# Kernel tuning notes

Hardware: AMD Instinct MI355X
Metric: run time of the kernel (lower is better)

Reference implementation:

```python
import jax, jax.numpy as jnp
import numpy as np

B, T, C, H = 4, 2048, 1024, 16

def setup_inputs() -> dict:
    key = jax.random.key(0)
    k1, k2, k3, k4, k5 = jax.random.split(key, 5)
    s = 1.0 / np.sqrt(C)
    return {
        "x": jax.random.normal(k1, (B, T, C), dtype=jnp.float32),
        "w_attn": jax.random.normal(k2, (C, 3 * C), dtype=jnp.float32) * s,
        "b_attn": jax.random.normal(k3, (3 * C,), dtype=jnp.float32) * 0.02,
        "w_proj": jax.random.normal(k4, (C, C), dtype=jnp.float32) * s,
        "b_proj": jax.random.normal(k5, (C,), dtype=jnp.float32) * 0.02,
    }

def reference(x, w_attn, b_attn, w_proj, b_proj):
    Bx, Tx, Cx = x.shape
    hd = Cx // H  # head_size
    qkv = x @ w_attn + b_attn                      # [B,T,3C]
    q, k, v = jnp.split(qkv, 3, axis=2)
    # [B,T,C] -> [B,H,T,hd]
    def heads(t):
        return t.reshape(Bx, Tx, H, hd).transpose(0, 2, 1, 3)
    q, k, v = heads(q), heads(k), heads(v)
    scale = hd ** -0.5
    scores = jnp.einsum("bhqd,bhkd->bhqk", q, k) * scale  # [B,H,T,T]
    causal = jnp.tril(jnp.ones((Tx, Tx), dtype=bool))
    scores = jnp.where(causal[None, None], scores, -jnp.inf)
    probs = jax.nn.softmax(scores, axis=-1)
    attn = jnp.einsum("bhqk,bhkd->bhqd", probs, v)  # [B,H,T,hd]
    attn = attn.transpose(0, 2, 1, 3).reshape(Bx, Tx, Cx)
    return attn @ w_proj + b_proj
```

## Files before the change

### kernel.cpp

```cpp
#include <hip/hip_runtime.h>
#include <hip/hip_bf16.h>

#define BATCH 4
#define TSEQ  2048
#define CDIM  1024
#define NHEAD 16
#define HDIM  64
#define C3    3072
#define MROWS (BATCH * TSEQ)

#define QSCALE 0.18033688011112f

typedef short bf16x8 __attribute__((ext_vector_type(8)));
typedef short short8 __attribute__((ext_vector_type(8)));
typedef __bf16 bf16v8 __attribute__((ext_vector_type(8)));
typedef float f32x4 __attribute__((ext_vector_type(4)));

#define AS1 __attribute__((address_space(1)))
#define AS3 __attribute__((address_space(3)))

__device__ __forceinline__ short f2bf(float x) {
    unsigned int u = __builtin_bit_cast(unsigned int, x);
    u += 0x7fffu + ((u >> 16) & 1u);
    return (short)(u >> 16);
}

__device__ __forceinline__ unsigned int cvtpk(float lo, float hi) {
    unsigned int r;
    asm("v_cvt_pk_bf16_f32 %0, %1, %2" : "=v"(r) : "v"(lo), "v"(hi));
    return r;
}

__device__ __forceinline__ f32x4 mfma16(bf16x8 a, bf16x8 b, f32x4 c) {
    return __builtin_amdgcn_mfma_f32_16x16x32_bf16(
        __builtin_bit_cast(bf16v8, a), __builtin_bit_cast(bf16v8, b), c, 0, 0, 0);
}

__global__ void f32_to_bf16_kernel(const float* __restrict__ in,
                                   short* __restrict__ out, int n8) {
    int i = blockIdx.x * blockDim.x + threadIdx.x;
    if (i >= n8) return;
    float4 a = ((const float4*)in)[2 * i];
    float4 b = ((const float4*)in)[2 * i + 1];
    short8 o;
    o[0] = f2bf(a.x); o[1] = f2bf(a.y); o[2] = f2bf(a.z); o[3] = f2bf(a.w);
    o[4] = f2bf(b.x); o[5] = f2bf(b.y); o[6] = f2bf(b.z); o[7] = f2bf(b.w);
    ((short8*)out)[i] = o;
}

__global__ void transpose_f32_bf16_kernel(const float* __restrict__ in,
                                          short* __restrict__ out,
                                          int K, int N, int qcols, float qs) {
    __shared__ float tile[32][33];
    const int n0 = blockIdx.x * 32, k0 = blockIdx.y * 32;
    const int tx = threadIdx.x, ty = threadIdx.y;
#pragma unroll
    for (int j = 0; j < 4; ++j)
        tile[ty + j * 8][tx] = in[(size_t)(k0 + ty + j * 8) * N + n0 + tx];
    __syncthreads();
#pragma unroll
    for (int j = 0; j < 4; ++j) {
        const int n = n0 + ty + j * 8;
        const float s = (n < qcols) ? qs : 1.0f;
        out[(size_t)n * K + k0 + tx] = f2bf(tile[tx][ty + j * 8] * s);
    }
}

template <typename OutT, int WAVES_M, int WAVES_N, int BN>
__global__ __launch_bounds__(512, 4) void gemm3_kernel(
    const short* __restrict__ A, const short* __restrict__ Bt,
    const float* __restrict__ bias, OutT* __restrict__ out,
    int M, int N, int K, int qcols, float qs) {
    constexpr int BM = 128;
    constexpr int MF = BM / (WAVES_M * 16);
    constexpr int NF = BN / (WAVES_N * 16);
    constexpr int BLOADS = BN / 128;
    __shared__ alignas(16) short Ab[3][BM * 32];
    __shared__ alignas(16) short Bb[3][BN * 32];

    const int tid = threadIdx.x;
    const int lane = tid & 63;
    const int w = tid >> 6;
    const int wm = w / WAVES_N;
    const int wn = w % WAVES_N;

    const int nwg = gridDim.x * gridDim.y;
    const int lid = blockIdx.y * gridDim.x + blockIdx.x;
    const int swz = (lid & 7) * (nwg >> 3) + (lid >> 3);
    const int m0 = (swz / gridDim.x) * BM;
    const int n0 = (swz % gridDim.x) * BN;

    const int NT = K >> 5;

    const int fr = lane & 15;
    const int ch = lane >> 4;

    f32x4 acc[MF][NF] = {};

    const int rA  = tid >> 2;
    const int lcA = (tid & 3) ^ ((rA >> 1) & 3);
    const short* gA = A + (size_t)(m0 + rA) * K + lcA * 8;
    const short* gB[BLOADS];
#pragma unroll
    for (int i = 0; i < BLOADS; ++i) {
        const int s = tid + i * 512;
        const int r = s >> 2;
        const int lc = (s & 3) ^ ((r >> 1) & 3);
        gB[i] = Bt + (size_t)(n0 + r) * K + lc * 8;
    }

    int aoff[MF], boff[NF];
#pragma unroll
    for (int f = 0; f < MF; ++f) {
        const int r = wm * (BM / WAVES_M) + f * 16 + fr;
        aoff[f] = r * 32 + (ch ^ ((r >> 1) & 3)) * 8;
    }
#pragma unroll
    for (int f = 0; f < NF; ++f) {
        const int r = wn * (BN / WAVES_N) + f * 16 + fr;
        boff[f] = r * 32 + (ch ^ ((r >> 1) & 3)) * 8;
    }

#define GSTAGE(buf, kt)                                                          \
    do {                                                                         \
        __builtin_amdgcn_global_load_lds((const AS1 void*)(gA + (kt)),           \
            (AS3 void*)&Ab[buf][w * 512], 16, 0, 0);                             \
        _Pragma("unroll")                                                        \
        for (int i = 0; i < BLOADS; ++i)                                         \
            __builtin_amdgcn_global_load_lds((const AS1 void*)(gB[i] + (kt)),    \
                (AS3 void*)&Bb[buf][i * 4096 + w * 512], 16, 0, 0);              \
    } while (0)

#define GITER(BUF, T)                                                            \
    do {                                                                         \
        if constexpr (BLOADS == 2) {                                             \
            asm volatile("s_waitcnt vmcnt(3)" ::: "memory");                     \
        } else {                                                                 \
            asm volatile("s_waitcnt vmcnt(2)" ::: "memory");                     \
        }                                                                        \
        __builtin_amdgcn_s_barrier();                                            \
        __builtin_amdgcn_sched_barrier(0);                                       \
        bf16x8 af[MF], bfv[NF];                                                  \
        _Pragma("unroll")                                                        \
        for (int f = 0; f < MF; ++f)                                             \
            af[f] = *(const bf16x8*)&Ab[BUF][aoff[f]];                           \
        _Pragma("unroll")                                                        \
        for (int f = 0; f < NF; ++f)                                             \
            bfv[f] = *(const bf16x8*)&Bb[BUF][boff[f]];                          \
        const int ktn = (((T) + 2 < NT) ? ((T) + 2) : 0) * 32;                   \
        GSTAGE((BUF + 2) % 3, ktn);                                              \
        _Pragma("unroll")                                                        \
        for (int mf = 0; mf < MF; ++mf)                                          \
            _Pragma("unroll")                                                    \
            for (int nf = 0; nf < NF; ++nf)                                      \
                acc[mf][nf] = mfma16(af[mf], bfv[nf], acc[mf][nf]);              \
    } while (0)

    GSTAGE(0, 0);
    GSTAGE(1, 32);

    int t = 0;
    for (; t + 3 <= NT; t += 3) {
        GITER(0, t);
        GITER(1, t + 1);
        GITER(2, t + 2);
    }
    if (t < NT) { GITER(0, t); ++t; }
    if (t < NT) { GITER(1, t); }
#undef GITER
#undef GSTAGE

    const int r0 = (lane >> 4) * 4;
    const int cn = lane & 15;
#pragma unroll
    for (int mf = 0; mf < MF; ++mf) {
#pragma unroll
        for (int nf = 0; nf < NF; ++nf) {
            const int col = n0 + wn * (BN / WAVES_N) + nf * 16 + cn;
            const float bv = bias[col] * ((col < qcols) ? qs : 1.0f);
#pragma unroll
            for (int r = 0; r < 4; ++r) {
                const int row = m0 + wm * (BM / WAVES_M) + mf * 16 + r0 + r;
                const float v = acc[mf][nf][r] + bv;
                if constexpr (sizeof(OutT) == 2)
                    out[(size_t)row * N + col] = (OutT)f2bf(v);
                else
                    out[(size_t)row * N + col] = (OutT)v;
            }
        }
    }
}

template <int BUF>
__device__ __forceinline__ void attn_iter(
    int KB, int niter, int qrow, int w, int cn, int g, int kg8,
    int krow, int kx0, int kx1, int skv, int sd0,
    const short* kgl, size_t ksrc, const short* vbase,
    short (*klds)[64 * 64], short (*vt)[64 * 72],
    const bf16x8 (&qf)[2][2], f32x4 (&ao)[2][4], f32x4 (&ao4)[2],
    const bf16x8& vones) {

    const int kvb = KB * 64;
    const bool pf = (KB + 1 < niter);

    bf16x8 r0, r1;
    if (pf) {
        r0 = *(const bf16x8*)(vbase + (size_t)(kvb + 64 + skv) * C3 + sd0);
        r1 = *(const bf16x8*)(vbase + (size_t)(kvb + 64 + skv + 1) * C3 + sd0);
        const short* kn = kgl + ksrc + (size_t)(kvb + 64) * C3;
        __builtin_amdgcn_global_load_lds((const AS1 void*)kn,
            (AS3 void*)&klds[BUF ^ 1][w * 512], 16, 0, 0);
        __builtin_amdgcn_global_load_lds((const AS1 void*)(kn + (size_t)32 * C3),
            (AS3 void*)&klds[BUF ^ 1][2048 + w * 512], 16, 0, 0);
    }

    if (kvb <= qrow + 31) {
        bf16x8 kf[4][2];
#pragma unroll
        for (int t = 0; t < 4; ++t) {
            const int rb = t * 1024 + krow;
            kf[t][0] = *(const bf16x8*)&klds[BUF][rb + kx0];
            kf[t][1] = *(const bf16x8*)&klds[BUF][rb + kx1];
        }

        bf16x8 vf[2][4];
#pragma unroll
        for (int c = 0; c < 2; ++c)
#pragma unroll
            for (int dt = 0; dt < 4; ++dt)
                vf[c][dt] = *(const bf16x8*)&vt[BUF][(dt * 16 + cn) * 72 + c * 32 + kg8];

#pragma unroll
        for (int qt = 0; qt < 2; ++qt) {
            const int qrow16 = qrow + qt * 16;

            f32x4 s[4] = {};
#pragma unroll
            for (int t = 0; t < 4; ++t) {
                s[t] = mfma16(kf[t][0], qf[qt][0], s[t]);
                s[t] = mfma16(kf[t][1], qf[qt][1], s[t]);
            }

            const bool maskIter = (kvb + 63 > qrow16);
            float p[4][4];
            if (maskIter) {
#pragma unroll
                for (int t = 0; t < 4; ++t)
#pragma unroll
                    for (int r = 0; r < 4; ++r) {
                        const int kv = kvb + t * 16 + 4 * g + r;
                        const int q  = qrow16 + cn;
                        float e = exp2f(s[t][r]);
                        p[t][r] = (kv > q) ? 0.f : e;
                    }
            } else {
#pragma unroll
                for (int t = 0; t < 4; ++t)
#pragma unroll
                    for (int r = 0; r < 4; ++r)
                        p[t][r] = exp2f(s[t][r]);
            }

            unsigned int wq[8];
#pragma unroll
            for (int t = 0; t < 4; ++t) {
                wq[t * 2 + 0] = cvtpk(p[t][0], p[t][1]);
                wq[t * 2 + 1] = cvtpk(p[t][2], p[t][3]);
            }

#pragma unroll
            for (int c = 0; c < 2; ++c) {
                union { unsigned int u[4]; bf16x8 v; } pu;
                unsigned int p0 = wq[4 * c + 0], p2 = wq[4 * c + 2];
                asm("v_permlane32_swap_b32 %0, %1" : "+v"(p0), "+v"(p2));
                asm("v_permlane16_swap_b32 %0, %1" : "+v"(p0), "+v"(p2));
                pu.u[0] = p0; pu.u[2] = p2;
                unsigned int p1 = wq[4 * c + 1], p3 = wq[4 * c + 3];
                asm("v_permlane32_swap_b32 %0, %1" : "+v"(p1), "+v"(p3));
                asm("v_permlane16_swap_b32 %0, %1" : "+v"(p1), "+v"(p3));
                pu.u[1] = p1; pu.u[3] = p3;
#pragma unroll
                for (int dt = 0; dt < 4; ++dt)
                    ao[qt][dt] = mfma16(pu.v, vf[c][dt], ao[qt][dt]);
                ao4[qt] = mfma16(pu.v, vones, ao4[qt]);
            }
        }
    }

    if (pf) {
#pragma unroll
        for (int i = 0; i < 8; ++i) {
            unsigned int pk = (unsigned short)r0[i] | ((unsigned int)(unsigned short)r1[i] << 16);
            *(unsigned int*)&vt[BUF ^ 1][(sd0 + i) * 72 + skv] = pk;
        }
    }
    __syncthreads();
}

__global__ __launch_bounds__(256) void attn_kernel(const short* __restrict__ qkv,
                                                   short* __restrict__ attn_out) {
    __shared__ short vt[2][64 * 72];
    __shared__ short klds[2][64 * 64];

    const int tid = threadIdx.x;
    const int lane = tid & 63;
    const int w = tid >> 6;

    const int bid = blockIdx.x;
    const int swz = (bid & 7) * 64 + (bid >> 3);
    const int bh = swz >> 3;
    const int pairp = swz & 7;
    const int b = bh >> 4;
    const int h = bh & 15;

    const size_t base = (size_t)b * TSEQ * C3 + (size_t)h * HDIM;
    const int cn = lane & 15;
    const int g = lane >> 4;
    const int kg8 = g * 8;

    const bf16x8 vones = {0x3F80, 0x3F80, 0x3F80, 0x3F80,
                          0x3F80, 0x3F80, 0x3F80, 0x3F80};

    const short* kgl = qkv + base + 1024;
    const size_t ksrc = (size_t)(w * 8 + (lane >> 3)) * C3 + ((lane & 7) ^ (lane >> 3)) * 8;
    const int cnl = cn & 7;
    const int krow = cn * 64;
    const int kx0 = ((g ^ cnl) * 8);
    const int kx1 = (((g ^ 4) ^ cnl) * 8);

    const int skv = (tid & 31) * 2;
    const int sd0 = (tid >> 5) * 8;
    const short* vbase = qkv + base + 2048;

    for (int pass = 0; pass < 2; ++pass) {
        const int qi = pass ? pairp : (15 - pairp);
        const int q0 = qi * 128;
        const int qrow = q0 + w * 32;
        const int niter = 2 * qi + 2;

        bf16x8 qf[2][2];
#pragma unroll
        for (int qt = 0; qt < 2; ++qt)
#pragma unroll
            for (int ks = 0; ks < 2; ++ks)
                qf[qt][ks] = *(const bf16x8*)(qkv + base +
                    (size_t)(qrow + qt * 16 + cn) * C3 + ks * 32 + kg8);

        f32x4 ao[2][4] = {};
        f32x4 ao4[2] = {};

        {
            __builtin_amdgcn_global_load_lds((const AS1 void*)(kgl + ksrc),
                                             (AS3 void*)&klds[0][w * 512], 16, 0, 0);
            __builtin_amdgcn_global_load_lds((const AS1 void*)(kgl + ksrc + (size_t)32 * C3),
                                             (AS3 void*)&klds[0][2048 + w * 512], 16, 0, 0);
            bf16x8 r0 = *(const bf16x8*)(vbase + (size_t)skv * C3 + sd0);
            bf16x8 r1 = *(const bf16x8*)(vbase + (size_t)(skv + 1) * C3 + sd0);
#pragma unroll
            for (int i = 0; i < 8; ++i) {
                unsigned int pk = (unsigned short)r0[i] | ((unsigned int)(unsigned short)r1[i] << 16);
                *(unsigned int*)&vt[0][(sd0 + i) * 72 + skv] = pk;
            }
        }
        __syncthreads();

        int kb = 0;
        for (; kb + 2 <= niter; kb += 2) {
            attn_iter<0>(kb,     niter, qrow, w, cn, g, kg8, krow, kx0, kx1,
                         skv, sd0, kgl, ksrc, vbase, klds, vt, qf, ao, ao4, vones);
            attn_iter<1>(kb + 1, niter, qrow, w, cn, g, kg8, krow, kx0, kx1,
                         skv, sd0, kgl, ksrc, vbase, klds, vt, qf, ao, ao4, vones);
        }

#pragma unroll
        for (int qt = 0; qt < 2; ++qt) {
#pragma unroll
            for (int r = 0; r < 4; ++r) {
                const float lr = 1.0f / ao4[qt][r];
                const int q = qrow + qt * 16 + 4 * g + r;
#pragma unroll
                for (int dt = 0; dt < 4; ++dt)
                    attn_out[(size_t)(b * TSEQ + q) * CDIM + h * HDIM + dt * 16 + cn] =
                        f2bf(ao[qt][dt][r] * lr);
            }
        }
        __syncthreads();
    }
}

extern "C" void kernel_launch(void* const* d_in, const int* in_sizes, int n_in,
                              void* d_out, int out_size, void* d_ws, size_t ws_size,
                              hipStream_t stream) {
    const float* x      = (const float*)d_in[0];
    const float* w_attn = (const float*)d_in[1];
    const float* b_attn = (const float*)d_in[2];
    const float* w_proj = (const float*)d_in[3];
    const float* b_proj = (const float*)d_in[4];
    float* out = (float*)d_out;

    char* ws = (char*)d_ws;
    short* x_bf   = (short*)ws;
    short* wqkvT  = (short*)(ws + (16u << 20));
    short* wprojT = (short*)(ws + (22u << 20));
    short* qkv    = (short*)(ws + (24u << 20));

    f32_to_bf16_kernel<<<(MROWS * CDIM / 8 + 255) / 256, 256, 0, stream>>>(x, x_bf, MROWS * CDIM / 8);
    transpose_f32_bf16_kernel<<<dim3(C3 / 32, CDIM / 32), dim3(32, 8), 0, stream>>>(
        w_attn, wqkvT, CDIM, C3, CDIM, QSCALE);
    transpose_f32_bf16_kernel<<<dim3(CDIM / 32, CDIM / 32), dim3(32, 8), 0, stream>>>(
        w_proj, wprojT, CDIM, CDIM, 0, 1.0f);

    gemm3_kernel<short, 2, 4, 256><<<dim3(C3 / 256, MROWS / 128), 512, 0, stream>>>(
        x_bf, wqkvT, b_attn, qkv, MROWS, C3, CDIM, CDIM, QSCALE);

    attn_kernel<<<dim3(512), 256, 0, stream>>>(qkv, x_bf);

    gemm3_kernel<float, 4, 2, 128><<<dim3(CDIM / 128, MROWS / 128), 512, 0, stream>>>(
        x_bf, wprojT, b_proj, out, MROWS, CDIM, CDIM, 0, 1.0f);
}
```

Baseline: 182.1 us.

## Split attention q-tile pairs into separate blocks with XCD-aware causal balancing

```diff
diff --git a/kernel.cpp b/kernel.cpp
--- a/kernel.cpp
+++ b/kernel.cpp
@@ -15,9 +15,16 @@
 typedef short short8 __attribute__((ext_vector_type(8)));
 typedef __bf16 bf16v8 __attribute__((ext_vector_type(8)));
 typedef float f32x4 __attribute__((ext_vector_type(4)));
+typedef unsigned int u32x4v __attribute__((ext_vector_type(4)));
 
 #define AS1 __attribute__((address_space(1)))
 #define AS3 __attribute__((address_space(3)))
+
+#if __has_builtin(__builtin_amdgcn_exp2f)
+#define EXP2F(x) __builtin_amdgcn_exp2f(x)
+#else
+#define EXP2F(x) exp2f(x)
+#endif
 
 __device__ __forceinline__ short f2bf(float x) {
     unsigned int u = __builtin_bit_cast(unsigned int, x);
@@ -34,6 +41,27 @@
 __device__ __forceinline__ f32x4 mfma16(bf16x8 a, bf16x8 b, f32x4 c) {
     return __builtin_amdgcn_mfma_f32_16x16x32_bf16(
         __builtin_bit_cast(bf16v8, a), __builtin_bit_cast(bf16v8, b), c, 0, 0, 0);
+}
+
+__device__ __forceinline__ void vpack_write(short* dst, const bf16x8& r0,
+                                            const bf16x8& r1, int skv, int sd0) {
+#if __has_builtin(__builtin_amdgcn_perm)
+    u32x4v a = __builtin_bit_cast(u32x4v, r0);
+    u32x4v b = __builtin_bit_cast(u32x4v, r1);
+#pragma unroll
+    for (int wd = 0; wd < 4; ++wd) {
+        unsigned int lo = __builtin_amdgcn_perm(b[wd], a[wd], 0x05040100u);
+        unsigned int hi = __builtin_amdgcn_perm(b[wd], a[wd], 0x07060302u);
+        *(unsigned int*)&dst[(sd0 + 2 * wd + 0) * 72 + skv] = lo;
+        *(unsigned int*)&dst[(sd0 + 2 * wd + 1) * 72 + skv] = hi;
+    }
+#else
+#pragma unroll
+    for (int i = 0; i < 8; ++i) {
+        unsigned int pk = (unsigned short)r0[i] | ((unsigned int)(unsigned short)r1[i] << 16);
+        *(unsigned int*)&dst[(sd0 + i) * 72 + skv] = pk;
+    }
+#endif
 }
 
 __global__ void f32_to_bf16_kernel(const float* __restrict__ in,
@@ -250,7 +278,7 @@
                     for (int r = 0; r < 4; ++r) {
                         const int kv = kvb + t * 16 + 4 * g + r;
                         const int q  = qrow16 + cn;
-                        float e = exp2f(s[t][r]);
+                        float e = EXP2F(s[t][r]);
                         p[t][r] = (kv > q) ? 0.f : e;
                     }
             } else {
@@ -258,7 +286,7 @@
                 for (int t = 0; t < 4; ++t)
 #pragma unroll
                     for (int r = 0; r < 4; ++r)
-                        p[t][r] = exp2f(s[t][r]);
+                        p[t][r] = EXP2F(s[t][r]);
             }
 
             unsigned int wq[8];
@@ -287,18 +315,12 @@
         }
     }
 
-    if (pf) {
-#pragma unroll
-        for (int i = 0; i < 8; ++i) {
-            unsigned int pk = (unsigned short)r0[i] | ((unsigned int)(unsigned short)r1[i] << 16);
-            *(unsigned int*)&vt[BUF ^ 1][(sd0 + i) * 72 + skv] = pk;
-        }
-    }
+    if (pf) vpack_write(vt[BUF ^ 1], r0, r1, skv, sd0);
     __syncthreads();
 }
 
-__global__ __launch_bounds__(256) void attn_kernel(const short* __restrict__ qkv,
-                                                   short* __restrict__ attn_out) {
+__global__ __launch_bounds__(256, 4) void attn_kernel(const short* __restrict__ qkv,
+                                                      short* __restrict__ attn_out) {
     __shared__ short vt[2][64 * 72];
     __shared__ short klds[2][64 * 64];
 
@@ -307,9 +329,12 @@
     const int w = tid >> 6;
 
     const int bid = blockIdx.x;
-    const int swz = (bid & 7) * 64 + (bid >> 3);
-    const int bh = swz >> 3;
-    const int pairp = swz & 7;
+    const int xcd = bid & 7;
+    const int cu  = (bid >> 3) & 31;
+    const int k   = bid >> 8;
+    const int j   = cu >> 3;
+    const int qi  = (k & 1) ? (15 - 2 * j - (k >> 1)) : (2 * j + (k >> 1));
+    const int bh  = xcd * 8 + (cu & 7);
     const int b = bh >> 4;
     const int h = bh & 15;
 
@@ -332,59 +357,51 @@
     const int sd0 = (tid >> 5) * 8;
     const short* vbase = qkv + base + 2048;
 
-    for (int pass = 0; pass < 2; ++pass) {
-        const int qi = pass ? pairp : (15 - pairp);
-        const int q0 = qi * 128;
-        const int qrow = q0 + w * 32;
-        const int niter = 2 * qi + 2;
-
-        bf16x8 qf[2][2];
-#pragma unroll
-        for (int qt = 0; qt < 2; ++qt)
-#pragma unroll
-            for (int ks = 0; ks < 2; ++ks)
-                qf[qt][ks] = *(const bf16x8*)(qkv + base +
-                    (size_t)(qrow + qt * 16 + cn) * C3 + ks * 32 + kg8);
-
-        f32x4 ao[2][4] = {};
-        f32x4 ao4[2] = {};
-
-        {
-            __builtin_amdgcn_global_load_lds((const AS1 void*)(kgl + ksrc),
-                                             (AS3 void*)&klds[0][w * 512], 16, 0, 0);
-            __builtin_amdgcn_global_load_lds((const AS1 void*)(kgl + ksrc + (size_t)32 * C3),
-                                             (AS3 void*)&klds[0][2048 + w * 512], 16, 0, 0);
-            bf16x8 r0 = *(const bf16x8*)(vbase + (size_t)skv * C3 + sd0);
-            bf16x8 r1 = *(const bf16x8*)(vbase + (size_t)(skv + 1) * C3 + sd0);
-#pragma unroll
-            for (int i = 0; i < 8; ++i) {
-                unsigned int pk = (unsigned short)r0[i] | ((unsigned int)(unsigned short)r1[i] << 16);
-                *(unsigned int*)&vt[0][(sd0 + i) * 72 + skv] = pk;
-            }
+    const int q0 = qi * 128;
+    const int qrow = q0 + w * 32;
+    const int niter = 2 * qi + 2;
+
+    bf16x8 qf[2][2];
+#pragma unroll
+    for (int qt = 0; qt < 2; ++qt)
+#pragma unroll
+        for (int ks = 0; ks < 2; ++ks)
+            qf[qt][ks] = *(const bf16x8*)(qkv + base +
+                (size_t)(qrow + qt * 16 + cn) * C3 + ks * 32 + kg8);
+
+    f32x4 ao[2][4] = {};
+    f32x4 ao4[2] = {};
+
+    {
+        __builtin_amdgcn_global_load_lds((const AS1 void*)(kgl + ksrc),
+                                         (AS3 void*)&klds[0][w * 512], 16, 0, 0);
+        __builtin_amdgcn_global_load_lds((const AS1 void*)(kgl + ksrc + (size_t)32 * C3),
+                                         (AS3 void*)&klds[0][2048 + w * 512], 16, 0, 0);
+        bf16x8 r0 = *(const bf16x8*)(vbase + (size_t)skv * C3 + sd0);
+        bf16x8 r1 = *(const bf16x8*)(vbase + (size_t)(skv + 1) * C3 + sd0);
+        vpack_write(vt[0], r0, r1, skv, sd0);
+    }
+    __syncthreads();
+
+    int kb = 0;
+    for (; kb + 2 <= niter; kb += 2) {
+        attn_iter<0>(kb,     niter, qrow, w, cn, g, kg8, krow, kx0, kx1,
+                     skv, sd0, kgl, ksrc, vbase, klds, vt, qf, ao, ao4, vones);
+        attn_iter<1>(kb + 1, niter, qrow, w, cn, g, kg8, krow, kx0, kx1,
+                     skv, sd0, kgl, ksrc, vbase, klds, vt, qf, ao, ao4, vones);
+    }
+
+#pragma unroll
+    for (int qt = 0; qt < 2; ++qt) {
+#pragma unroll
+        for (int r = 0; r < 4; ++r) {
+            const float lr = 1.0f / ao4[qt][r];
+            const int q = qrow + qt * 16 + 4 * g + r;
+#pragma unroll
+            for (int dt = 0; dt < 4; ++dt)
+                attn_out[(size_t)(b * TSEQ + q) * CDIM + h * HDIM + dt * 16 + cn] =
+                    f2bf(ao[qt][dt][r] * lr);
         }
-        __syncthreads();
-
-        int kb = 0;
-        for (; kb + 2 <= niter; kb += 2) {
-            attn_iter<0>(kb,     niter, qrow, w, cn, g, kg8, krow, kx0, kx1,
-                         skv, sd0, kgl, ksrc, vbase, klds, vt, qf, ao, ao4, vones);
-            attn_iter<1>(kb + 1, niter, qrow, w, cn, g, kg8, krow, kx0, kx1,
-                         skv, sd0, kgl, ksrc, vbase, klds, vt, qf, ao, ao4, vones);
-        }
-
-#pragma unroll
-        for (int qt = 0; qt < 2; ++qt) {
-#pragma unroll
-            for (int r = 0; r < 4; ++r) {
-                const float lr = 1.0f / ao4[qt][r];
-                const int q = qrow + qt * 16 + 4 * g + r;
-#pragma unroll
-                for (int dt = 0; dt < 4; ++dt)
-                    attn_out[(size_t)(b * TSEQ + q) * CDIM + h * HDIM + dt * 16 + cn] =
-                        f2bf(ao[qt][dt][r] * lr);
-            }
-        }
-        __syncthreads();
     }
 }
 
@@ -413,7 +430,7 @@
     gemm3_kernel<short, 2, 4, 256><<<dim3(C3 / 256, MROWS / 128), 512, 0, stream>>>(
         x_bf, wqkvT, b_attn, qkv, MROWS, C3, CDIM, CDIM, QSCALE);
 
-    attn_kernel<<<dim3(512), 256, 0, stream>>>(qkv, x_bf);
+    attn_kernel<<<dim3(1024), 256, 0, stream>>>(qkv, x_bf);
 
     gemm3_kernel<float, 4, 2, 128><<<dim3(CDIM / 128, MROWS / 128), 512, 0, stream>>>(
         x_bf, wprojT, b_proj, out, MROWS, CDIM, CDIM, 0, 1.0f);
```

After: 394.3 us. 117% more time.
